# Kernel tuning notes

Measured on AMD Instinct MI355X. Metric: run time of the kernel, lower is better.

Reference implementation:

```python
import jax, jax.numpy as jnp
import numpy as np

E4M3_MAX = 448.0
IGNORE = -1000.0
ROTARY_BASE = 10000.0


def quant_dequant_e4m3(w):
    """Emulate per-tensor FP8 E4M3 quantize->dequantize (3 mantissa bits, max 448)."""
    amax = jnp.max(jnp.abs(w))
    scale = E4M3_MAX / jnp.maximum(amax, 1e-12)
    v = w * scale
    a = jnp.abs(v)
    # exponent clipped to E4M3 range (min normal exp -6, max 8)
    e = jnp.clip(jnp.floor(jnp.log2(jnp.maximum(a, 1e-30))), -6.0, 8.0)
    step = jnp.exp2(e - 3.0)  # 3 mantissa bits
    q = jnp.clip(jnp.round(v / step) * step, -E4M3_MAX, E4M3_MAX)
    return (q / scale).astype(w.dtype)


def rotary_sin_cos(rotary_dim, n_ctx):
    pos = jnp.arange(n_ctx, dtype=jnp.float32)
    dim = jnp.arange(rotary_dim // 2, dtype=jnp.float32)
    inv_freq = ROTARY_BASE ** (-dim / (rotary_dim / 2))
    ang = pos[:, None] * inv_freq[None, :]            # [n_ctx, rotary_dim//2]
    ang = jnp.concatenate([ang, ang], axis=-1)        # [n_ctx, rotary_dim]
    return jnp.sin(ang), jnp.cos(ang)


def apply_rotary(x, sin, cos, rotary_dim):
    # x: [B, S, H, Dh]; rotate first rotary_dim dims with rotate-half convention
    S = x.shape[1]
    x_rot, x_pass = x[..., :rotary_dim], x[..., rotary_dim:]
    half = rotary_dim // 2
    x_flip = jnp.concatenate([-x_rot[..., half:], x_rot[..., :half]], axis=-1)
    c = cos[:S][None, :, None, :]
    s = sin[:S][None, :, None, :]
    out = x_rot * c + x_flip * s
    return jnp.concatenate([out, x_pass], axis=-1) if rotary_dim < x.shape[-1] else out


def setup_inputs() -> dict:
    key = jax.random.key(0)
    ks = jax.random.split(key, 8)
    B, S, D, H, Dh = 2, 2048, 1024, 16, 64
    return {
        "query_input": jax.random.normal(ks[0], (B, S, D), jnp.float32),
        "key_input": jax.random.normal(ks[1], (B, S, D), jnp.float32),
        "value_input": jax.random.normal(ks[2], (B, S, D), jnp.float32),
        "W_Q": jax.random.normal(ks[3], (H, D, Dh), jnp.float32) * 0.02,
        "W_K": jax.random.normal(ks[4], (H, D, Dh), jnp.float32) * 0.02,
        "W_V": jax.random.normal(ks[5], (H, D, Dh), jnp.float32) * 0.02,
        "W_O": jax.random.normal(ks[6], (H, Dh, D), jnp.float32) * 0.02,
        "b_Q": jnp.zeros((H, Dh), jnp.float32),
        "b_K": jnp.zeros((H, Dh), jnp.float32),
        "b_V": jnp.zeros((H, Dh), jnp.float32),
        "b_O": jnp.zeros((D,), jnp.float32),
    }


def reference(query_input, key_input, value_input, W_Q, W_K, W_V, W_O, b_Q, b_K, b_V, b_O):
    B, S, D = query_input.shape
    H, _, Dh = W_Q.shape
    rotary_dim = Dh
    attn_scale = jnp.sqrt(jnp.asarray(Dh, jnp.float32))

    # FP8-quantized QKV weights/biases (E4M3 quant-dequant emulation)
    Wq = quant_dequant_e4m3(W_Q)
    Wk = quant_dequant_e4m3(W_K)
    Wv = quant_dequant_e4m3(W_V)
    bq = quant_dequant_e4m3(b_Q)
    bk = quant_dequant_e4m3(b_K)
    bv = quant_dequant_e4m3(b_V)

    q = jnp.einsum("bsd,hde->bshe", query_input, Wq) + bq  # [B,S,H,Dh]
    k = jnp.einsum("bsd,hde->bshe", key_input, Wk) + bk
    v = jnp.einsum("bsd,hde->bshe", value_input, Wv) + bv

    sin, cos = rotary_sin_cos(rotary_dim, S)
    q = apply_rotary(q, sin, cos, rotary_dim)
    k = apply_rotary(k, sin, cos, rotary_dim)

    scores = jnp.einsum("bqhe,bkhe->bhqk", q, k) / attn_scale  # [B,H,S,S]
    causal = jnp.tril(jnp.ones((S, S), bool))
    scores = jnp.where(causal[None, None], scores, IGNORE)
    pattern = jax.nn.softmax(scores, axis=-1)

    z = jnp.einsum("bhqk,bkhe->bqhe", pattern, v)             # [B,S,H,Dh]
    out = jnp.einsum("bqhe,hed->bqd", z, W_O) + b_O           # [B,S,D]
    return out
```

## Files before the change

kernel.cpp:

```cpp
#include <hip/hip_runtime.h>
#include <math.h>


typedef __attribute__((ext_vector_type(8))) short bf16x8;
typedef __attribute__((ext_vector_type(16))) float f32x16;
typedef __attribute__((ext_vector_type(4))) float f32x4;
typedef __attribute__((ext_vector_type(4))) float f4;

#define E4M3_MAX 448.0f

__device__ inline float bf2f(ushort u) { return __uint_as_float(((unsigned)u) << 16); }
__device__ inline ushort f2bf(float f) {
  unsigned u = __float_as_uint(f);
  return (ushort)((u + 0x7FFF + ((u >> 16) & 1)) >> 16);
}
__device__ inline unsigned pack2bf(float a, float b) {
  unsigned ua = __float_as_uint(a), ub = __float_as_uint(b);
  return ((ua + 0x8000u) >> 16) | ((ub + 0x8000u) & 0xFFFF0000u);
}

__device__ __forceinline__ void gll16(const ushort* g, ushort* l) {
  __builtin_amdgcn_global_load_lds(
      (const __attribute__((address_space(1))) unsigned int*)g,
      (__attribute__((address_space(3))) unsigned int*)l, 16, 0, 0);
}

__global__ void zero16_kernel(float* p) {
  if (threadIdx.x < 16) p[threadIdx.x] = 0.0f;
}

__global__ __launch_bounds__(256) void amax6_kernel(const float* __restrict__ p0,
                                                    const float* __restrict__ p1,
                                                    const float* __restrict__ p2,
                                                    const float* __restrict__ p3,
                                                    const float* __restrict__ p4,
                                                    const float* __restrict__ p5,
                                                    float* __restrict__ amax) {
  int y = blockIdx.y;
  const float* src = (y == 0) ? p0 : (y == 1) ? p1 : (y == 2) ? p2 : (y == 3) ? p3 : (y == 4) ? p4 : p5;
  int n = (y < 3) ? 1048576 : 1024;
  float m = 0.0f;
  int stride = gridDim.x * 256;
  for (int i = blockIdx.x * 256 + threadIdx.x; i < n; i += stride)
    m = fmaxf(m, fabsf(src[i]));
  #pragma unroll
  for (int off = 32; off > 0; off >>= 1)
    m = fmaxf(m, __shfl_xor(m, off));
  __shared__ float wred[4];
  if ((threadIdx.x & 63) == 0) wred[threadIdx.x >> 6] = m;
  __syncthreads();
  if (threadIdx.x == 0) {
    m = fmaxf(fmaxf(wred[0], wred[1]), fmaxf(wred[2], wred[3]));
    atomicMax((unsigned int*)(amax + y), __float_as_uint(m));
  }
}

__device__ inline float qdq_qval(float w, float amax) {
  float scale = E4M3_MAX / fmaxf(amax, 1e-12f);
  float v = w * scale;
  float a = fmaxf(fabsf(v), 1e-30f);
  int ex;
  (void)frexpf(a, &ex);
  float e = fminf(fmaxf((float)(ex - 1), -6.0f), 8.0f);
  float step = exp2f(e - 3.0f);
  float q = rintf(v / step) * step;
  return fminf(fmaxf(q, -E4M3_MAX), E4M3_MAX);
}

__global__ void qvec3_kernel(const float* __restrict__ b0, const float* __restrict__ b1,
                             const float* __restrict__ b2, const float* __restrict__ amax,
                             float* __restrict__ o0, float* __restrict__ o1,
                             float* __restrict__ o2) {
  int y = blockIdx.y;
  const float* b = (y == 0) ? b0 : (y == 1) ? b1 : b2;
  float* o = (y == 0) ? o0 : (y == 1) ? o1 : o2;
  float am = amax[3 + y];
  int idx = blockIdx.x * blockDim.x + threadIdx.x;
  if (idx < 1024) {
    float q = qdq_qval(b[idx], am);
    o[idx] = q * (fmaxf(am, 1e-12f) * (1.0f / E4M3_MAX));
  }
}

__global__ __launch_bounds__(256) void quant_repack_bt3(const float* __restrict__ W0,
                                                        const float* __restrict__ W1,
                                                        const float* __restrict__ W2,
                                                        const float* __restrict__ amaxp,
                                                        ushort* __restrict__ o0,
                                                        ushort* __restrict__ o1,
                                                        ushort* __restrict__ o2) {
  int z = blockIdx.z;
  const float* W = (z == 0) ? W0 : (z == 1) ? W1 : W2;
  ushort* Bt = (z == 0) ? o0 : (z == 1) ? o1 : o2;
  float amax = amaxp[z];
  __shared__ float tile[64][65];
  int d0 = blockIdx.x * 64, hh = blockIdx.y;
  int tid = threadIdx.x;
  int e = tid & 63, dd = tid >> 6;
  #pragma unroll
  for (int p = 0; p < 16; p++)
    tile[dd + p * 4][e] = W[(size_t)hh * 65536 + (size_t)(d0 + dd + p * 4) * 64 + e];
  __syncthreads();
  int d = tid & 63, ee = tid >> 6;
  #pragma unroll
  for (int p = 0; p < 16; p++) {
    int e2 = ee + p * 4;
    Bt[(size_t)(hh * 64 + e2) * 1024 + d0 + d] = f2bf(qdq_qval(tile[d][e2], amax));
  }
}

__global__ __launch_bounds__(256) void wo_trans(const float* __restrict__ W,
                                               ushort* __restrict__ Bt) {
  __shared__ float tile[64][65];
  int d0 = blockIdx.x * 64, he0 = blockIdx.y * 64;
  int tid = threadIdx.x;
  int dcol = tid & 63, hr = tid >> 6;
  #pragma unroll
  for (int p = 0; p < 16; p++)
    tile[hr + p * 4][dcol] = W[(size_t)(he0 + hr + p * 4) * 1024 + d0 + dcol];
  __syncthreads();
  int hcol = tid & 63, dr = tid >> 6;
  #pragma unroll
  for (int p = 0; p < 16; p++)
    Bt[(size_t)(d0 + dr + p * 4) * 1024 + he0 + hcol] = f2bf(tile[hcol][dr + p * 4]);
}

__global__ __launch_bounds__(256) void cvt3_kernel(const float* __restrict__ i0,
                                                   const float* __restrict__ i1,
                                                   const float* __restrict__ i2,
                                                   ushort* __restrict__ o0,
                                                   ushort* __restrict__ o1,
                                                   ushort* __restrict__ o2) {
  int y = blockIdx.y;
  const float* in = (y == 0) ? i0 : (y == 1) ? i1 : i2;
  ushort* out = (y == 0) ? o0 : (y == 1) ? o1 : o2;
  int i = blockIdx.x * 256 + threadIdx.x;
  f4 v = *(const f4*)(in + (size_t)i * 4);
  uint2 o;
  o.x = (unsigned)f2bf(v[0]) | ((unsigned)f2bf(v[1]) << 16);
  o.y = (unsigned)f2bf(v[2]) | ((unsigned)f2bf(v[3]) << 16);
  *(uint2*)(out + (size_t)i * 4) = o;
}

template <int QUANT, int TN>
__device__ __forceinline__ void gemm_body(const ushort* __restrict__ A,
                                          const ushort* __restrict__ Bt,
                                          const float* __restrict__ bias, float s_inv,
                                          ushort* __restrict__ outb, float* __restrict__ outf,
                                          int bx, int by, ushort* As, ushort* Bs) {
  const int K = 1024, N = 1024;
  const int JF = TN / 32;
  int tid = threadIdx.x;
  int w = tid >> 6, lane = tid & 63, quad = lane >> 4, l16 = lane & 15;
  int wm = w & 1, wn = w >> 1;
  int row0 = by * 128, col0 = bx * TN;
  f32x4 acc[4][4] = {};

  for (int k0 = 0; k0 < K; k0 += 32) {
    __syncthreads();
    {
      int u = tid;
      gll16(&A[(size_t)(row0 + (u >> 2)) * K + k0 + (u & 3) * 8], &As[u * 8]);
      u = tid + 256;
      gll16(&A[(size_t)(row0 + (u >> 2)) * K + k0 + (u & 3) * 8], &As[u * 8]);
      u = tid;
      gll16(&Bt[(size_t)(col0 + (u >> 2)) * K + k0 + (u & 3) * 8], &Bs[u * 8]);
      if (TN == 128) {
        u = tid + 256;
        gll16(&Bt[(size_t)(col0 + (u >> 2)) * K + k0 + (u & 3) * 8], &Bs[u * 8]);
      }
    }
    __syncthreads();
    bf16x8 af[4], bfr[JF];
    #pragma unroll
    for (int i = 0; i < 4; i++)
      af[i] = *(const bf16x8*)&As[(wm * 64 + i * 16 + l16) * 32 + quad * 8];
    #pragma unroll
    for (int j = 0; j < JF; j++)
      bfr[j] = *(const bf16x8*)&Bs[(wn * (TN / 2) + j * 16 + l16) * 32 + quad * 8];
    #pragma unroll
    for (int i = 0; i < 4; i++)
      #pragma unroll
      for (int j = 0; j < JF; j++)
        acc[i][j] = __builtin_amdgcn_mfma_f32_16x16x32_bf16(af[i], bfr[j], acc[i][j], 0, 0, 0);
  }

  #pragma unroll
  for (int j = 0; j < JF; j++) {
    int col = col0 + wn * (TN / 2) + j * 16 + l16;
    float bv = bias[col];
    #pragma unroll
    for (int i = 0; i < 4; i++) {
      int row = row0 + wm * 64 + i * 16 + quad * 4;
      #pragma unroll
      for (int r = 0; r < 4; r++) {
        float v = acc[i][j][r] * s_inv + bv;
        if (QUANT) outb[(size_t)(row + r) * N + col] = f2bf(v);
        else       outf[(size_t)(row + r) * N + col] = v;
      }
    }
  }
}

__global__ __launch_bounds__(256) void gemm3_qkv(const ushort* __restrict__ xq,
                                                 const ushort* __restrict__ xk,
                                                 const ushort* __restrict__ xv,
                                                 const ushort* __restrict__ wq,
                                                 const ushort* __restrict__ wk,
                                                 const ushort* __restrict__ wv,
                                                 const float* __restrict__ bq,
                                                 const float* __restrict__ bk,
                                                 const float* __restrict__ bv,
                                                 const float* __restrict__ amax,
                                                 ushort* __restrict__ oq,
                                                 ushort* __restrict__ ok,
                                                 ushort* __restrict__ ov) {
  __shared__ ushort As[4096], Bs[4096];
  int z = blockIdx.z;
  const ushort* A  = (z == 0) ? xq : (z == 1) ? xk : xv;
  const ushort* Bt = (z == 0) ? wq : (z == 1) ? wk : wv;
  const float* bias = (z == 0) ? bq : (z == 1) ? bk : bv;
  ushort* out = (z == 0) ? oq : (z == 1) ? ok : ov;
  float s_inv = fmaxf(amax[z], 1e-12f) * (1.0f / E4M3_MAX);
  gemm_body<1, 128>(A, Bt, bias, s_inv, out, nullptr, blockIdx.x, blockIdx.y, As, Bs);
}

__global__ __launch_bounds__(256) void gemm_wo(const ushort* __restrict__ A,
                                               const ushort* __restrict__ Bt,
                                               const float* __restrict__ bias,
                                               float* __restrict__ out) {
  __shared__ ushort As[4096], Bs[2048];
  gemm_body<0, 64>(A, Bt, bias, 1.0f, nullptr, out, blockIdx.x, blockIdx.y, As, Bs);
}

__global__ __launch_bounds__(256) void rotary_bf(ushort* qb, ushort* kb) {
  int bs = blockIdx.x;
  int s = bs & 2047;
  int tid = threadIdx.x;
  int e = tid & 63, w = tid >> 6;
  int j = e & 31;
  float inv_freq = exp2f((float)j * (-13.287712379549449f / 32.0f));
  float ang = (float)s * inv_freq;
  float c = cosf(ang), sn = sinf(ang);
  float sgn = (e < 32) ? -1.0f : 1.0f;
  size_t base = (size_t)bs * 1024;
  #pragma unroll
  for (int i = 0; i < 4; i++) {
    int h = w + i * 4;
    size_t idx = base + (size_t)h * 64 + e;
    float x = bf2f(qb[idx]);
    float xp = __shfl_xor(x, 32);
    qb[idx] = f2bf(x * c + sgn * xp * sn);
    float y = bf2f(kb[idx]);
    float yp = __shfl_xor(y, 32);
    kb[idx] = f2bf(y * c + sgn * yp * sn);
  }
}

__global__ __launch_bounds__(256) void v_trans(const ushort* __restrict__ v,
                                              ushort* __restrict__ vT) {
  __shared__ ushort tile[64][72];
  int s0 = blockIdx.x * 64, h = blockIdx.y, b = blockIdx.z;
  int tid = threadIdx.x;
  int e = tid & 63, sr = tid >> 6;
  #pragma unroll
  for (int p = 0; p < 16; p++)
    tile[sr + p * 4][e] = v[(size_t)(b * 2048 + s0 + sr + p * 4) * 1024 + h * 64 + e];
  __syncthreads();
  int sc = tid & 63, er = tid >> 6;
  #pragma unroll
  for (int p = 0; p < 16; p++)
    vT[(size_t)((b * 16 + h) * 64 + er + p * 4) * 2048 + s0 + sc] = tile[sc][er + p * 4];
}

__global__ __launch_bounds__(256, 2) void flash_mfma4(const ushort* __restrict__ qb,
                                                      const ushort* __restrict__ kb,
                                                      const ushort* __restrict__ vT,
                                                      ushort* __restrict__ zb) {
  int qt = (int)gridDim.x - 1 - (int)blockIdx.x;
  int h = blockIdx.y, b = blockIdx.z;
  int tid = threadIdx.x;
  int w = tid >> 6, lane = tid & 63, h2 = lane >> 5, l31 = lane & 31;
  __shared__ ushort sbuf[8192 + 9216];
  ushort* Ks = sbuf;
  ushort* Vs = sbuf + 4096;
  ushort* P2 = sbuf + 8192;

  const int q0 = qt * 128;
  const int qg = q0 + w * 32 + l31;
  const int qrow = w * 32 + l31;
  size_t qbase = ((size_t)(b * 2048 + qg)) * 1024 + (size_t)h * 64;
  bf16x8 qf[4];
  #pragma unroll
  for (int ck = 0; ck < 4; ck++)
    qf[ck] = *(const bf16x8*)&qb[qbase + ck * 16 + h2 * 8];

  f32x16 accO[2] = {};
  float mrun = -INFINITY, lrun = 0.0f;
  const float CE = 0.125f;

  const int u0 = tid, u1 = tid + 256;
  const int r0 = u0 >> 3, c0 = u0 & 7, r1 = u1 >> 3, c1 = u1 & 7;
  const int sw0 = (c0 ^ (r0 & 7)) * 8, sw1 = (c1 ^ (r1 & 7)) * 8;
  const ushort* ksrc0 = kb + ((size_t)(b * 2048 + r0)) * 1024 + (size_t)h * 64 + c0 * 8;
  const ushort* ksrc1 = kb + ((size_t)(b * 2048 + r1)) * 1024 + (size_t)h * 64 + c1 * 8;
  const ushort* vsrc0 = vT + ((size_t)((b * 16 + h) * 64 + r0)) * 2048 + c0 * 8;
  const ushort* vsrc1 = vT + ((size_t)((b * 16 + h) * 64 + r1)) * 2048 + c1 * 8;

  int ktmax = 2 * qt + 1;
  uint4 kc0 = *(const uint4*)ksrc0;
  uint4 kc1 = *(const uint4*)ksrc1;
  uint4 vc0 = *(const uint4*)vsrc0;
  uint4 vc1 = *(const uint4*)vsrc1;

  for (int kt = 0; kt <= ktmax; kt++) {
    __syncthreads();
    *(uint4*)&Ks[r0 * 64 + sw0] = kc0;
    *(uint4*)&Ks[r1 * 64 + sw1] = kc1;
    *(uint4*)&Vs[r0 * 64 + sw0] = vc0;
    *(uint4*)&Vs[r1 * 64 + sw1] = vc1;
    __syncthreads();
    if (kt < ktmax) {
      kc0 = *(const uint4*)(ksrc0 + (size_t)(kt + 1) * 65536);
      kc1 = *(const uint4*)(ksrc1 + (size_t)(kt + 1) * 65536);
      vc0 = *(const uint4*)(vsrc0 + (kt + 1) * 64);
      vc1 = *(const uint4*)(vsrc1 + (kt + 1) * 64);
    }

    bool active = (kt * 64 <= q0 + w * 32 + 31);
    if (active) {
      f32x16 sc[2] = {};
      #pragma unroll
      for (int mf = 0; mf < 2; mf++) {
        int row = mf * 32 + l31;
        int s8 = row & 7;
        #pragma unroll
        for (int ck = 0; ck < 4; ck++) {
          bf16x8 ka = *(const bf16x8*)&Ks[row * 64 + (((2 * ck + h2) ^ s8) * 8)];
          sc[mf] = __builtin_amdgcn_mfma_f32_32x32x16_bf16(ka, qf[ck], sc[mf], 0, 0, 0);
        }
      }

      if (kt * 64 + 63 > q0 + w * 32) {
        #pragma unroll
        for (int mf = 0; mf < 2; mf++)
          #pragma unroll
          for (int i = 0; i < 16; i++) {
            int kv = kt * 64 + mf * 32 + (i & 3) + 8 * (i >> 2) + 4 * h2;
            sc[mf][i] = (kv > qg) ? -8000.0f : sc[mf][i];
          }
      }

      float tm = sc[0][0];
      #pragma unroll
      for (int i = 1; i < 16; i++) tm = fmaxf(tm, sc[0][i]);
      #pragma unroll
      for (int i = 0; i < 16; i++) tm = fmaxf(tm, sc[1][i]);
      tm = fmaxf(tm, __shfl_xor(tm, 32));
      float mnew = fmaxf(mrun, tm);
      float alpha = __expf((mrun - mnew) * CE);
      float p[2][16];
      float rs = 0.0f;
      #pragma unroll
      for (int mf = 0; mf < 2; mf++)
        #pragma unroll
        for (int i = 0; i < 16; i++) {
          float pv = __expf((sc[mf][i] - mnew) * CE);
          p[mf][i] = pv;
          rs += pv;
        }
      rs += __shfl_xor(rs, 32);
      lrun = lrun * alpha + rs;
      mrun = mnew;
      #pragma unroll
      for (int mf = 0; mf < 2; mf++)
        #pragma unroll
        for (int i = 0; i < 16; i++) accO[mf][i] *= alpha;

      #pragma unroll
      for (int mf = 0; mf < 2; mf++)
        #pragma unroll
        for (int m = 0; m < 4; m++) {
          uint2 w2;
          w2.x = pack2bf(p[mf][4 * m + 0], p[mf][4 * m + 1]);
          w2.y = pack2bf(p[mf][4 * m + 2], p[mf][4 * m + 3]);
          *(uint2*)&P2[qrow * 72 + 32 * mf + 8 * m + 4 * h2] = w2;
        }
    }
    __syncthreads();
    if (active) {
      #pragma unroll
      for (int ck = 0; ck < 4; ck++) {
        bf16x8 pB = *(const bf16x8*)&P2[qrow * 72 + ck * 16 + h2 * 8];
        #pragma unroll
        for (int mf = 0; mf < 2; mf++) {
          int row = mf * 32 + l31;
          bf16x8 va = *(const bf16x8*)&Vs[row * 64 + (((2 * ck + h2) ^ (row & 7)) * 8)];
          accO[mf] = __builtin_amdgcn_mfma_f32_32x32x16_bf16(va, pB, accO[mf], 0, 0, 0);
        }
      }
    }
  }

  float inv = 1.0f / lrun;
  __syncthreads();
  ushort* Osb = P2;
  #pragma unroll
  for (int mf = 0; mf < 2; mf++)
    #pragma unroll
    for (int m = 0; m < 4; m++) {
      int e0 = 32 * mf + 8 * m + 4 * h2;
      float a0 = accO[mf][4 * m + 0] * inv, a1 = accO[mf][4 * m + 1] * inv;
      float a2 = accO[mf][4 * m + 2] * inv, a3 = accO[mf][4 * m + 3] * inv;
      *(unsigned*)&Osb[qrow * 72 + e0] = pack2bf(a0, a1);
      *(unsigned*)&Osb[qrow * 72 + e0 + 2] = pack2bf(a2, a3);
    }
  __syncthreads();
  size_t obase = ((size_t)(b * 2048 + q0)) * 1024 + (size_t)h * 64;
  #pragma unroll
  for (int i = 0; i < 4; i++) {
    int u = tid + i * 256;
    int r = u >> 3, blk = u & 7;
    *(uint4*)&zb[obase + (size_t)r * 1024 + blk * 8] = *(const uint4*)&Osb[r * 72 + blk * 8];
  }
}

extern "C" void kernel_launch(void* const* d_in, const int* in_sizes, int n_in,
                              void* d_out, int out_size, void* d_ws, size_t ws_size,
                              hipStream_t stream) {
  const float* Xq  = (const float*)d_in[0];
  const float* Xk  = (const float*)d_in[1];
  const float* Xv  = (const float*)d_in[2];
  const float* W_Q = (const float*)d_in[3];
  const float* W_K = (const float*)d_in[4];
  const float* W_V = (const float*)d_in[5];
  const float* W_O = (const float*)d_in[6];
  const float* b_Q = (const float*)d_in[7];
  const float* b_K = (const float*)d_in[8];
  const float* b_V = (const float*)d_in[9];
  const float* b_O = (const float*)d_in[10];
  float* out = (float*)d_out;

  char* base = (char*)d_ws;
  float*  amax = (float*)(base + 0);
  float*  bq   = (float*)(base + 4096);
  float*  bk   = (float*)(base + 8192);
  float*  bv   = (float*)(base + 12288);
  ushort* wq   = (ushort*)(base + 16384);
  ushort* wk   = (ushort*)(base + 16384 + 2097152);
  ushort* wv   = (ushort*)(base + 16384 + 2u * 2097152);
  ushort* woT  = (ushort*)(base + 16384 + 3u * 2097152);
  ushort* xq   = (ushort*)(base + 8404992);
  ushort* xk   = (ushort*)(base + 16793600);
  ushort* xv   = (ushort*)(base + 25182208);
  ushort* qbf  = (ushort*)(base + 33570816);
  ushort* kbf  = (ushort*)(base + 41959424);
  ushort* vbf  = (ushort*)(base + 50348032);
  ushort* vT   = xq;
  ushort* zbf  = xk;

  zero16_kernel<<<1, 64, 0, stream>>>(amax);
  dim3 agrid(64, 6);
  amax6_kernel<<<agrid, 256, 0, stream>>>(W_Q, W_K, W_V, b_Q, b_K, b_V, amax);

  dim3 rgrid(16, 16, 3);
  quant_repack_bt3<<<rgrid, 256, 0, stream>>>(W_Q, W_K, W_V, amax, wq, wk, wv);
  dim3 qvgrid(4, 3);
  qvec3_kernel<<<qvgrid, 256, 0, stream>>>(b_Q, b_K, b_V, amax, bq, bk, bv);
  dim3 wgrid(16, 16);
  wo_trans<<<wgrid, 256, 0, stream>>>(W_O, woT);
  dim3 cgrid(4096, 3);
  cvt3_kernel<<<cgrid, 256, 0, stream>>>(Xq, Xk, Xv, xq, xk, xv);

  dim3 g3(8, 32, 3);
  gemm3_qkv<<<g3, 256, 0, stream>>>(xq, xk, xv, wq, wk, wv, bq, bk, bv, amax,
                                    qbf, kbf, vbf);

  rotary_bf<<<4096, 256, 0, stream>>>(qbf, kbf);

  dim3 vgrid(32, 16, 2);
  v_trans<<<vgrid, 256, 0, stream>>>(vbf, vT);

  dim3 fgrid(16, 16, 2);
  flash_mfma4<<<fgrid, 256, 0, stream>>>(qbf, kbf, vT, zbf);

  dim3 wog(16, 32);
  gemm_wo<<<wog, 256, 0, stream>>>(zbf, woT, b_O, out);
}
```

Before: 276.3 us.

## Fuse V transpose into QKV GEMM epilogue and pair causal tiles in flash kernel

The V projection GEMM now writes its output directly in transposed [b,h,e,s] layout, so the separate v_trans kernel and its extra pass over V are gone. The flash attention kernel has each block process two query tiles (qt and 15-qt), balancing causal work across half as many blocks. The P staging stride changes to 68, with split 8-byte reads, to reduce LDS bank conflicts. The amax grid is also widened. Risks are uncoalesced 8-byte scattered stores in the GEMM epilogue and lower parallelism in the attention grid.

Result: no change. 280.8 us (+1.6%).

```diff
diff --git a/kernel.cpp b/kernel.cpp
--- a/kernel.cpp
+++ b/kernel.cpp
@@ -142,7 +142,7 @@
   *(uint2*)(out + (size_t)i * 4) = o;
 }
 
-template <int QUANT, int TN>
+template <int MODE, int TN>
 __device__ __forceinline__ void gemm_body(const ushort* __restrict__ A,
                                           const ushort* __restrict__ Bt,
                                           const float* __restrict__ bias, float s_inv,
@@ -192,11 +192,20 @@
     #pragma unroll
     for (int i = 0; i < 4; i++) {
       int row = row0 + wm * 64 + i * 16 + quad * 4;
-      #pragma unroll
-      for (int r = 0; r < 4; r++) {
-        float v = acc[i][j][r] * s_inv + bv;
-        if (QUANT) outb[(size_t)(row + r) * N + col] = f2bf(v);
-        else       outf[(size_t)(row + r) * N + col] = v;
+      if (MODE == 2) {
+        float v0 = acc[i][j][0] * s_inv + bv, v1 = acc[i][j][1] * s_inv + bv;
+        float v2 = acc[i][j][2] * s_inv + bv, v3 = acc[i][j][3] * s_inv + bv;
+        uint2 o;
+        o.x = (unsigned)f2bf(v0) | ((unsigned)f2bf(v1) << 16);
+        o.y = (unsigned)f2bf(v2) | ((unsigned)f2bf(v3) << 16);
+        *(uint2*)&outb[((size_t)((row >> 11) * 1024 + col)) * 2048 + (row & 2047)] = o;
+      } else {
+        #pragma unroll
+        for (int r = 0; r < 4; r++) {
+          float v = acc[i][j][r] * s_inv + bv;
+          if (MODE == 1) outb[(size_t)(row + r) * N + col] = f2bf(v);
+          else           outf[(size_t)(row + r) * N + col] = v;
+        }
       }
     }
   }
@@ -214,15 +223,18 @@
                                                  const float* __restrict__ amax,
                                                  ushort* __restrict__ oq,
                                                  ushort* __restrict__ ok,
-                                                 ushort* __restrict__ ov) {
+                                                 ushort* __restrict__ ovT) {
   __shared__ ushort As[4096], Bs[4096];
   int z = blockIdx.z;
   const ushort* A  = (z == 0) ? xq : (z == 1) ? xk : xv;
   const ushort* Bt = (z == 0) ? wq : (z == 1) ? wk : wv;
   const float* bias = (z == 0) ? bq : (z == 1) ? bk : bv;
-  ushort* out = (z == 0) ? oq : (z == 1) ? ok : ov;
   float s_inv = fmaxf(amax[z], 1e-12f) * (1.0f / E4M3_MAX);
-  gemm_body<1, 128>(A, Bt, bias, s_inv, out, nullptr, blockIdx.x, blockIdx.y, As, Bs);
+  if (z == 2)
+    gemm_body<2, 128>(A, Bt, bias, s_inv, ovT, nullptr, blockIdx.x, blockIdx.y, As, Bs);
+  else
+    gemm_body<1, 128>(A, Bt, bias, s_inv, (z == 0) ? oq : ok, nullptr,
+                      blockIdx.x, blockIdx.y, As, Bs);
 }
 
 __global__ __launch_bounds__(256) void gemm_wo(const ushort* __restrict__ A,
@@ -257,27 +269,12 @@
   }
 }
 
-__global__ __launch_bounds__(256) void v_trans(const ushort* __restrict__ v,
-                                              ushort* __restrict__ vT) {
-  __shared__ ushort tile[64][72];
-  int s0 = blockIdx.x * 64, h = blockIdx.y, b = blockIdx.z;
-  int tid = threadIdx.x;
-  int e = tid & 63, sr = tid >> 6;
-  #pragma unroll
-  for (int p = 0; p < 16; p++)
-    tile[sr + p * 4][e] = v[(size_t)(b * 2048 + s0 + sr + p * 4) * 1024 + h * 64 + e];
-  __syncthreads();
-  int sc = tid & 63, er = tid >> 6;
-  #pragma unroll
-  for (int p = 0; p < 16; p++)
-    vT[(size_t)((b * 16 + h) * 64 + er + p * 4) * 2048 + s0 + sc] = tile[sc][er + p * 4];
-}
-
-__global__ __launch_bounds__(256, 2) void flash_mfma4(const ushort* __restrict__ qb,
+#define P2S 68
+__global__ __launch_bounds__(256, 2) void flash_mfma5(const ushort* __restrict__ qb,
                                                       const ushort* __restrict__ kb,
                                                       const ushort* __restrict__ vT,
                                                       ushort* __restrict__ zb) {
-  int qt = (int)gridDim.x - 1 - (int)blockIdx.x;
+  int pidx = blockIdx.x;
   int h = blockIdx.y, b = blockIdx.z;
   int tid = threadIdx.x;
   int w = tid >> 6, lane = tid & 63, h2 = lane >> 5, l31 = lane & 31;
@@ -286,19 +283,6 @@
   ushort* Vs = sbuf + 4096;
   ushort* P2 = sbuf + 8192;
 
-  const int q0 = qt * 128;
-  const int qg = q0 + w * 32 + l31;
-  const int qrow = w * 32 + l31;
-  size_t qbase = ((size_t)(b * 2048 + qg)) * 1024 + (size_t)h * 64;
-  bf16x8 qf[4];
-  #pragma unroll
-  for (int ck = 0; ck < 4; ck++)
-    qf[ck] = *(const bf16x8*)&qb[qbase + ck * 16 + h2 * 8];
-
-  f32x16 accO[2] = {};
-  float mrun = -INFINITY, lrun = 0.0f;
-  const float CE = 0.125f;
-
   const int u0 = tid, u1 = tid + 256;
   const int r0 = u0 >> 3, c0 = u0 & 7, r1 = u1 >> 3, c1 = u1 & 7;
   const int sw0 = (c0 ^ (r0 & 7)) * 8, sw1 = (c1 ^ (r1 & 7)) * 8;
@@ -307,121 +291,142 @@
   const ushort* vsrc0 = vT + ((size_t)((b * 16 + h) * 64 + r0)) * 2048 + c0 * 8;
   const ushort* vsrc1 = vT + ((size_t)((b * 16 + h) * 64 + r1)) * 2048 + c1 * 8;
 
-  int ktmax = 2 * qt + 1;
-  uint4 kc0 = *(const uint4*)ksrc0;
-  uint4 kc1 = *(const uint4*)ksrc1;
-  uint4 vc0 = *(const uint4*)vsrc0;
-  uint4 vc1 = *(const uint4*)vsrc1;
-
-  for (int kt = 0; kt <= ktmax; kt++) {
-    __syncthreads();
-    *(uint4*)&Ks[r0 * 64 + sw0] = kc0;
-    *(uint4*)&Ks[r1 * 64 + sw1] = kc1;
-    *(uint4*)&Vs[r0 * 64 + sw0] = vc0;
-    *(uint4*)&Vs[r1 * 64 + sw1] = vc1;
-    __syncthreads();
-    if (kt < ktmax) {
-      kc0 = *(const uint4*)(ksrc0 + (size_t)(kt + 1) * 65536);
-      kc1 = *(const uint4*)(ksrc1 + (size_t)(kt + 1) * 65536);
-      vc0 = *(const uint4*)(vsrc0 + (kt + 1) * 64);
-      vc1 = *(const uint4*)(vsrc1 + (kt + 1) * 64);
-    }
-
-    bool active = (kt * 64 <= q0 + w * 32 + 31);
-    if (active) {
-      f32x16 sc[2] = {};
-      #pragma unroll
-      for (int mf = 0; mf < 2; mf++) {
-        int row = mf * 32 + l31;
-        int s8 = row & 7;
-        #pragma unroll
-        for (int ck = 0; ck < 4; ck++) {
-          bf16x8 ka = *(const bf16x8*)&Ks[row * 64 + (((2 * ck + h2) ^ s8) * 8)];
-          sc[mf] = __builtin_amdgcn_mfma_f32_32x32x16_bf16(ka, qf[ck], sc[mf], 0, 0, 0);
-        }
-      }
-
-      if (kt * 64 + 63 > q0 + w * 32) {
-        #pragma unroll
-        for (int mf = 0; mf < 2; mf++)
-          #pragma unroll
-          for (int i = 0; i < 16; i++) {
-            int kv = kt * 64 + mf * 32 + (i & 3) + 8 * (i >> 2) + 4 * h2;
-            sc[mf][i] = (kv > qg) ? -8000.0f : sc[mf][i];
-          }
-      }
-
-      float tm = sc[0][0];
-      #pragma unroll
-      for (int i = 1; i < 16; i++) tm = fmaxf(tm, sc[0][i]);
-      #pragma unroll
-      for (int i = 0; i < 16; i++) tm = fmaxf(tm, sc[1][i]);
-      tm = fmaxf(tm, __shfl_xor(tm, 32));
-      float mnew = fmaxf(mrun, tm);
-      float alpha = __expf((mrun - mnew) * CE);
-      float p[2][16];
-      float rs = 0.0f;
-      #pragma unroll
-      for (int mf = 0; mf < 2; mf++)
-        #pragma unroll
-        for (int i = 0; i < 16; i++) {
-          float pv = __expf((sc[mf][i] - mnew) * CE);
-          p[mf][i] = pv;
-          rs += pv;
-        }
-      rs += __shfl_xor(rs, 32);
-      lrun = lrun * alpha + rs;
-      mrun = mnew;
-      #pragma unroll
-      for (int mf = 0; mf < 2; mf++)
-        #pragma unroll
-        for (int i = 0; i < 16; i++) accO[mf][i] *= alpha;
-
-      #pragma unroll
-      for (int mf = 0; mf < 2; mf++)
-        #pragma unroll
-        for (int m = 0; m < 4; m++) {
-          uint2 w2;
-          w2.x = pack2bf(p[mf][4 * m + 0], p[mf][4 * m + 1]);
-          w2.y = pack2bf(p[mf][4 * m + 2], p[mf][4 * m + 3]);
-          *(uint2*)&P2[qrow * 72 + 32 * mf + 8 * m + 4 * h2] = w2;
-        }
-    }
-    __syncthreads();
-    if (active) {
-      #pragma unroll
-      for (int ck = 0; ck < 4; ck++) {
-        bf16x8 pB = *(const bf16x8*)&P2[qrow * 72 + ck * 16 + h2 * 8];
+  const float CE = 0.125f;
+  const int qrow = w * 32 + l31;
+
+  #pragma unroll 1
+  for (int t = 0; t < 2; t++) {
+    const int qt = (t == 0) ? (15 - pidx) : pidx;
+    const int q0 = qt * 128;
+    const int qg = q0 + qrow;
+    size_t qbase = ((size_t)(b * 2048 + qg)) * 1024 + (size_t)h * 64;
+    bf16x8 qf[4];
+    #pragma unroll
+    for (int ck = 0; ck < 4; ck++)
+      qf[ck] = *(const bf16x8*)&qb[qbase + ck * 16 + h2 * 8];
+
+    f32x16 accO[2] = {};
+    float mrun = -INFINITY, lrun = 0.0f;
+
+    int ktmax = 2 * qt + 1;
+    uint4 kc0 = *(const uint4*)ksrc0;
+    uint4 kc1 = *(const uint4*)ksrc1;
+    uint4 vc0 = *(const uint4*)vsrc0;
+    uint4 vc1 = *(const uint4*)vsrc1;
+
+    for (int kt = 0; kt <= ktmax; kt++) {
+      __syncthreads();
+      *(uint4*)&Ks[r0 * 64 + sw0] = kc0;
+      *(uint4*)&Ks[r1 * 64 + sw1] = kc1;
+      *(uint4*)&Vs[r0 * 64 + sw0] = vc0;
+      *(uint4*)&Vs[r1 * 64 + sw1] = vc1;
+      __syncthreads();
+      if (kt < ktmax) {
+        kc0 = *(const uint4*)(ksrc0 + (size_t)(kt + 1) * 65536);
+        kc1 = *(const uint4*)(ksrc1 + (size_t)(kt + 1) * 65536);
+        vc0 = *(const uint4*)(vsrc0 + (kt + 1) * 64);
+        vc1 = *(const uint4*)(vsrc1 + (kt + 1) * 64);
+      }
+
+      bool active = (kt * 64 <= q0 + w * 32 + 31);
+      if (active) {
+        f32x16 sc[2] = {};
         #pragma unroll
         for (int mf = 0; mf < 2; mf++) {
           int row = mf * 32 + l31;
-          bf16x8 va = *(const bf16x8*)&Vs[row * 64 + (((2 * ck + h2) ^ (row & 7)) * 8)];
-          accO[mf] = __builtin_amdgcn_mfma_f32_32x32x16_bf16(va, pB, accO[mf], 0, 0, 0);
+          int s8 = row & 7;
+          #pragma unroll
+          for (int ck = 0; ck < 4; ck++) {
+            bf16x8 ka = *(const bf16x8*)&Ks[row * 64 + (((2 * ck + h2) ^ s8) * 8)];
+            sc[mf] = __builtin_amdgcn_mfma_f32_32x32x16_bf16(ka, qf[ck], sc[mf], 0, 0, 0);
+          }
         }
+
+        if (kt * 64 + 63 > q0 + w * 32) {
+          #pragma unroll
+          for (int mf = 0; mf < 2; mf++)
+            #pragma unroll
+            for (int i = 0; i < 16; i++) {
+              int kv = kt * 64 + mf * 32 + (i & 3) + 8 * (i >> 2) + 4 * h2;
+              sc[mf][i] = (kv > qg) ? -8000.0f : sc[mf][i];
+            }
+        }
+
+        float tm = sc[0][0];
+        #pragma unroll
+        for (int i = 1; i < 16; i++) tm = fmaxf(tm, sc[0][i]);
+        #pragma unroll
+        for (int i = 0; i < 16; i++) tm = fmaxf(tm, sc[1][i]);
+        tm = fmaxf(tm, __shfl_xor(tm, 32));
+        float mnew = fmaxf(mrun, tm);
+        float alpha = __expf((mrun - mnew) * CE);
+        float p[2][16];
+        float rs = 0.0f;
+        #pragma unroll
+        for (int mf = 0; mf < 2; mf++)
+          #pragma unroll
+          for (int i = 0; i < 16; i++) {
+            float pv = __expf((sc[mf][i] - mnew) * CE);
+            p[mf][i] = pv;
+            rs += pv;
+          }
+        rs += __shfl_xor(rs, 32);
+        lrun = lrun * alpha + rs;
+        mrun = mnew;
+        #pragma unroll
+        for (int mf = 0; mf < 2; mf++)
+          #pragma unroll
+          for (int i = 0; i < 16; i++) accO[mf][i] *= alpha;
+
+        #pragma unroll
+        for (int mf = 0; mf < 2; mf++)
+          #pragma unroll
+          for (int m = 0; m < 4; m++) {
+            uint2 w2;
+            w2.x = pack2bf(p[mf][4 * m + 0], p[mf][4 * m + 1]);
+            w2.y = pack2bf(p[mf][4 * m + 2], p[mf][4 * m + 3]);
+            *(uint2*)&P2[qrow * P2S + 32 * mf + 8 * m + 4 * h2] = w2;
+          }
+      }
+      __syncthreads();
+      if (active) {
+        #pragma unroll
+        for (int ck = 0; ck < 4; ck++) {
+          uint2 lo = *(const uint2*)&P2[qrow * P2S + ck * 16 + h2 * 8];
+          uint2 hi = *(const uint2*)&P2[qrow * P2S + ck * 16 + h2 * 8 + 4];
+          uint4 pb4 = {lo.x, lo.y, hi.x, hi.y};
+          bf16x8 pB = *(bf16x8*)&pb4;
+          #pragma unroll
+          for (int mf = 0; mf < 2; mf++) {
+            int row = mf * 32 + l31;
+            bf16x8 va = *(const bf16x8*)&Vs[row * 64 + (((2 * ck + h2) ^ (row & 7)) * 8)];
+            accO[mf] = __builtin_amdgcn_mfma_f32_32x32x16_bf16(va, pB, accO[mf], 0, 0, 0);
+          }
+        }
       }
     }
-  }
-
-  float inv = 1.0f / lrun;
-  __syncthreads();
-  ushort* Osb = P2;
-  #pragma unroll
-  for (int mf = 0; mf < 2; mf++)
-    #pragma unroll
-    for (int m = 0; m < 4; m++) {
-      int e0 = 32 * mf + 8 * m + 4 * h2;
-      float a0 = accO[mf][4 * m + 0] * inv, a1 = accO[mf][4 * m + 1] * inv;
-      float a2 = accO[mf][4 * m + 2] * inv, a3 = accO[mf][4 * m + 3] * inv;
-      *(unsigned*)&Osb[qrow * 72 + e0] = pack2bf(a0, a1);
-      *(unsigned*)&Osb[qrow * 72 + e0 + 2] = pack2bf(a2, a3);
+
+    float inv = 1.0f / lrun;
+    __syncthreads();
+    ushort* Osb = P2;
+    #pragma unroll
+    for (int mf = 0; mf < 2; mf++)
+      #pragma unroll
+      for (int m = 0; m < 4; m++) {
+        int e0 = 32 * mf + 8 * m + 4 * h2;
+        float a0 = accO[mf][4 * m + 0] * inv, a1 = accO[mf][4 * m + 1] * inv;
+        float a2 = accO[mf][4 * m + 2] * inv, a3 = accO[mf][4 * m + 3] * inv;
+        *(unsigned*)&Osb[qrow * 72 + e0] = pack2bf(a0, a1);
+        *(unsigned*)&Osb[qrow * 72 + e0 + 2] = pack2bf(a2, a3);
+      }
+    __syncthreads();
+    size_t obase = ((size_t)(b * 2048 + q0)) * 1024 + (size_t)h * 64;
+    #pragma unroll
+    for (int i = 0; i < 4; i++) {
+      int u = tid + i * 256;
+      int r = u >> 3, blk = u & 7;
+      *(uint4*)&zb[obase + (size_t)r * 1024 + blk * 8] = *(const uint4*)&Osb[r * 72 + blk * 8];
     }
-  __syncthreads();
-  size_t obase = ((size_t)(b * 2048 + q0)) * 1024 + (size_t)h * 64;
-  #pragma unroll
-  for (int i = 0; i < 4; i++) {
-    int u = tid + i * 256;
-    int r = u >> 3, blk = u & 7;
-    *(uint4*)&zb[obase + (size_t)r * 1024 + blk * 8] = *(const uint4*)&Osb[r * 72 + blk * 8];
   }
 }
 
@@ -455,12 +460,11 @@
   ushort* xv   = (ushort*)(base + 25182208);
   ushort* qbf  = (ushort*)(base + 33570816);
   ushort* kbf  = (ushort*)(base + 41959424);
-  ushort* vbf  = (ushort*)(base + 50348032);
-  ushort* vT   = xq;
+  ushort* vT   = (ushort*)(base + 50348032);
   ushort* zbf  = xk;
 
   zero16_kernel<<<1, 64, 0, stream>>>(amax);
-  dim3 agrid(64, 6);
+  dim3 agrid(256, 6);
   amax6_kernel<<<agrid, 256, 0, stream>>>(W_Q, W_K, W_V, b_Q, b_K, b_V, amax);
 
   dim3 rgrid(16, 16, 3);
@@ -474,15 +478,12 @@
 
   dim3 g3(8, 32, 3);
   gemm3_qkv<<<g3, 256, 0, stream>>>(xq, xk, xv, wq, wk, wv, bq, bk, bv, amax,
-                                    qbf, kbf, vbf);
+                                    qbf, kbf, vT);
 
   rotary_bf<<<4096, 256, 0, stream>>>(qbf, kbf);
 
-  dim3 vgrid(32, 16, 2);
-  v_trans<<<vgrid, 256, 0, stream>>>(vbf, vT);
-
-  dim3 fgrid(16, 16, 2);
-  flash_mfma4<<<fgrid, 256, 0, stream>>>(qbf, kbf, vT, zbf);
+  dim3 fgrid(8, 16, 2);
+  flash_mfma5<<<fgrid, 256, 0, stream>>>(qbf, kbf, vT, zbf);
 
   dim3 wog(16, 32);
   gemm_wo<<<wog, 256, 0, stream>>>(zbf, woT, b_O, out);
```
